# Optimization experiments

Hardware: AMD Instinct MI355X
Metric: run time of the kernel (lower is better)

## Reference

```python
import jax, jax.numpy as jnp
import numpy as np

B, V, FIN, H = 200, 40, 16, 128
NSW = 12          # switch edges
NE = 40           # regular edges
M = NE + NSW      # 52 total edges
MLP_HID = 1024
OUT = M + V + NSW # 104


def _build_graph():
    rng = np.random.default_rng(0)
    pairs = set()
    while len(pairs) < M:
        i, j = map(int, rng.integers(0, V, 2))
        if i < j:
            pairs.add((i, j))
    pairs = sorted(pairs)
    reg = np.array(pairs[:NE], np.int64)   # (NE,2)
    sw = np.array(pairs[NE:], np.int64)    # (NSW,2) row-major sorted, matches torch.nonzero order
    edges = np.concatenate([reg, sw], 0)   # switch edges last, matching graph_topo layout
    A = np.zeros((V, M), np.float32)
    A[edges[:, 0], np.arange(M)] = 1.0
    A[edges[:, 1], np.arange(M)] = -1.0
    return reg, sw, A


def setup_inputs():
    key = jax.random.key(0)
    ks = jax.random.split(key, 16)
    reg, sw, A = _build_graph()
    ei = jnp.broadcast_to(jnp.asarray(reg.T)[None], (B, 2, NE))
    si = jnp.broadcast_to(jnp.asarray(sw.T)[None], (B, 2, NSW))

    def w(k, shp, fan):
        return jax.random.normal(k, shp, jnp.float32) / np.sqrt(fan)

    return {
        'x_mod': jax.random.normal(ks[0], (B, V, FIN), jnp.float32),
        'ei': ei, 'si': si, 'A_inc': jnp.asarray(A),
        'embed': w(ks[1], (2, FIN), 1.0),
        'WU0': w(ks[2], (FIN, H), FIN), 'WV0': w(ks[3], (FIN, H), FIN),
        'WA0': w(ks[4], (FIN, H), FIN), 'WB0': w(ks[5], (FIN, H), FIN),
        'WC0': w(ks[6], (FIN, H), FIN),
        'WU1': w(ks[7], (H, H), H), 'WV1': w(ks[8], (H, H), H),
        'WA1': w(ks[9], (H, H), H), 'WB1': w(ks[10], (H, H), H),
        'WC1': w(ks[11], (H, H), H),
        'W1': w(ks[12], ((NSW + V) * H, MLP_HID), (NSW + V) * H),
        'b1': jnp.zeros((MLP_HID,), jnp.float32),
        'W2': w(ks[13], (MLP_HID, OUT), MLP_HID),
        'b2': jnp.zeros((OUT,), jnp.float32),
    }


def _layer(x, s, adj, smask, WU, WV, WA, WB, WC, residual):
    Ux = x @ WU
    Vx = x @ WV
    # gate features over dense VxV switch grid: e_ij = A s_ij + B x_i + C x_j
    e = jnp.einsum('bijf,fh->bijh', s, WA) + (x @ WB)[:, :, None, :] + (x @ WC)[:, None, :, :]
    gates = jax.nn.sigmoid(e) * smask[..., None]
    msg_edges = jnp.einsum('bij,bjh->bih', adj, Vx)   # regular-edge aggregation
    msg_sw = jnp.einsum('bijh,bjh->bih', gates, Vx)   # gated switch aggregation
    xh = jax.nn.relu(Ux + msg_edges + msg_sw)
    sh = jax.nn.relu(e)
    if residual:
        xh = x + xh
        sh = s + sh
    return xh, sh


def reference(x_mod, ei, si, A_inc, embed, WU0, WV0, WA0, WB0, WC0,
              WU1, WV1, WA1, WB1, WC1, W1, b1, W2, b2):
    i_sw, j_sw = si[0, 0], si[0, 1]   # switch indices (shared across batch)
    i_e, j_e = ei[0, 0], ei[0, 1]
    S = jnp.zeros((V, V), bool).at[i_sw, j_sw].set(True)   # upper-tri switch mask
    smask = jnp.broadcast_to(S, (B, V, V)).astype(x_mod.dtype)
    s0 = embed[S.astype(jnp.int32)]                        # (V,V,FIN) edge embedding
    s = jnp.broadcast_to(s0[None], (B, V, V, FIN))
    adj1 = jnp.zeros((V, V), x_mod.dtype).at[i_e, j_e].set(1.0)
    adj = jnp.broadcast_to((adj1 + adj1.T)[None], (B, V, V))
    x, s = _layer(x_mod, s, adj, smask, WU0, WV0, WA0, WB0, WC0, residual=False)
    x, s = _layer(x, s, adj, smask, WU1, WV1, WA1, WB1, WC1, residual=True)
    switches = s[:, i_sw, j_sw, :]                         # (B,NSW,H) irregular gather (torch.nonzero path)
    mlp_in = jnp.concatenate([switches.reshape(B, -1), x.reshape(B, -1)], axis=1)
    out = jax.nn.relu(mlp_in @ W1 + b1) @ W2 + b2          # (B,OUT)
    p_switch = jax.nn.sigmoid(out[:, -NSW:])
    graph_topo = jnp.ones((B, M), out.dtype).at[:, M - NSW:].set(p_switch)
    v = out[:, M:M + V].at[:, 0].set(1.0)
    p_fc = graph_topo * out[:, :M]
    q_fc = graph_topo * (v @ A_inc)                        # per-edge voltage difference flow
    pg = x_mod[:, :, 0] + jnp.einsum('vm,bm->bv', A_inc, p_fc)  # power balance completion
    qg = x_mod[:, :, 1] + jnp.einsum('vm,bm->bv', A_inc, q_fc)
    z = jnp.concatenate([p_fc, v, graph_topo], axis=1)     # (B, 2M+V)
    zc = jnp.concatenate([q_fc, pg, qg], axis=1)           # (B, M+2V)
    return z, zc
```

## Files before the change

### kernel.cpp

```cpp
#include <hip/hip_runtime.h>
#include <math.h>

#define B       200
#define V       40
#define FIN     16
#define H       128
#define NSW     12
#define NE      40
#define M       52
#define MLP_HID 1024
#define OUTD    104
#define MLP_IN  6656
#define ZDIM    144
#define ZCDIM   132
#define NCH     13
#define X1LD    136
#define MAXD    16

typedef __attribute__((ext_vector_type(8))) short bf16x8;
typedef __attribute__((ext_vector_type(4))) float f32x4;

__device__ __forceinline__ float sigmoidf(float x) {
    return 1.0f / (1.0f + expf(-x));
}
__device__ __forceinline__ unsigned short f2b(float x) {
    unsigned int u = __float_as_uint(x);
    u += 0x7fffu + ((u >> 16) & 1u);
    return (unsigned short)(u >> 16);
}
__device__ __forceinline__ float b2f(unsigned short s) {
    return __uint_as_float(((unsigned int)s) << 16);
}

__global__ __launch_bounds__(256) void k_prep(
        const float* __restrict__ WU0, const float* __restrict__ WV0,
        const float* __restrict__ WB0, const float* __restrict__ WC0,
        const float* __restrict__ WU1, const float* __restrict__ WV1,
        const float* __restrict__ WB1, const float* __restrict__ WC1,
        const float* __restrict__ WA1, const float* __restrict__ W2,
        unsigned short* __restrict__ W0t, unsigned short* __restrict__ Wt640,
        unsigned short* __restrict__ W2t) {
    int bx = blockIdx.x, tid = threadIdx.x;
    if (bx < 64) {
        int o0 = bx * 2048 + tid * 8;
#pragma unroll
        for (int i = 0; i < 8; ++i) {
            int o = o0 + i; int col = o >> 10, k = o & 1023;
            W2t[o] = (col < OUTD) ? f2b(W2[(size_t)k * OUTD + col]) : (unsigned short)0;
        }
    } else if (bx < 104) {
        int o0 = (bx - 64) * 2048 + tid * 8;
#pragma unroll
        for (int i = 0; i < 8; ++i) {
            int o = o0 + i; int col = o >> 7, f = o & 127;
            int m = col >> 7, hh = col & 127;
            const float* Ws = (m == 0) ? WU1 : (m == 1) ? WV1 : (m == 2) ? WB1
                            : (m == 3) ? WC1 : WA1;
            Wt640[o] = f2b(Ws[f * H + hh]);
        }
    } else {
        int o0 = (bx - 104) * 2048 + tid * 8;
#pragma unroll
        for (int i = 0; i < 8; ++i) {
            int o = o0 + i; int col = o >> 5, k = o & 31;
            int m = col >> 7, hh = col & 127;
            const float* Ws = (m == 0) ? WU0 : (m == 1) ? WV0 : (m == 2) ? WB0 : WC0;
            W0t[o] = (k < FIN) ? f2b(Ws[k * H + hh]) : (unsigned short)0;
        }
    }
}

__global__ __launch_bounds__(512) void k_gnn(const float* __restrict__ x,
        const int* __restrict__ ei, const int* __restrict__ si,
        const float* __restrict__ embed, const float* __restrict__ WA0,
        const unsigned short* __restrict__ W0t,
        const unsigned short* __restrict__ Wt640,
        unsigned short* __restrict__ Abf) {
    int b = blockIdx.x, tid = threadIdx.x;
    __shared__ unsigned short xb[48 * 40];
    __shared__ unsigned short uvbc[V * 512];
    __shared__ unsigned short x1l[64 * X1LD];
    __shared__ float gL[NSW * H];
    __shared__ float sA1l[NSW * H];
    __shared__ int   nbr[V][MAXD];
    __shared__ int   deg[V];

    int h = tid & 127, sub = tid >> 7;
    int lane = tid & 63, wv = tid >> 6;
    int lr = lane & 15, lk = lane >> 4;
    int n0w = wv * 64;

    for (int o = tid; o < 48 * 32; o += 512) {
        int r = o >> 5, k = o & 31;
        float v = (r < V && k < FIN) ? x[(size_t)b * V * FIN + r * FIN + k] : 0.f;
        xb[r * 40 + k] = f2b(v);
    }
    if (tid < V) deg[tid] = 0;
    for (int o = tid; o < 12 * 128; o += 512) {
        int rr = o >> 7;
        int row = (rr < 8) ? 40 + rr : 60 + (rr - 8);
        x1l[row * X1LD + (o & 127)] = 0;
    }
    __syncthreads();

    if (tid < NE) {
        int i = ei[tid], j = ei[NE + tid];
        int p = atomicAdd(&deg[i], 1); if (p < MAXD) nbr[i][p] = j;
        int q = atomicAdd(&deg[j], 1); if (q < MAXD) nbr[j][q] = i;
    } else if (tid < NE + NSW) {
        int k = tid - NE;
        int i = si[k], j = si[NSW + k];
        int p = atomicAdd(&deg[i], 1); if (p < MAXD) nbr[i][p] = j | ((k + 1) << 8);
    }
    {
        f32x4 acc[3][4];
#pragma unroll
        for (int rf = 0; rf < 3; ++rf)
#pragma unroll
            for (int cf = 0; cf < 4; ++cf) acc[rf][cf] = (f32x4){0.f, 0.f, 0.f, 0.f};
        int kseg = lk * 8;
        bf16x8 a0 = *(const bf16x8*)&xb[lr * 40 + kseg];
        bf16x8 a1 = *(const bf16x8*)&xb[(16 + lr) * 40 + kseg];
        bf16x8 a2 = *(const bf16x8*)&xb[(32 + lr) * 40 + kseg];
#pragma unroll
        for (int cf = 0; cf < 4; ++cf) {
            bf16x8 bf = *(const bf16x8*)&W0t[(n0w + cf * 16 + lr) * 32 + kseg];
            acc[0][cf] = __builtin_amdgcn_mfma_f32_16x16x32_bf16(a0, bf, acc[0][cf], 0, 0, 0);
            acc[1][cf] = __builtin_amdgcn_mfma_f32_16x16x32_bf16(a1, bf, acc[1][cf], 0, 0, 0);
            acc[2][cf] = __builtin_amdgcn_mfma_f32_16x16x32_bf16(a2, bf, acc[2][cf], 0, 0, 0);
        }
#pragma unroll
        for (int rf = 0; rf < 3; ++rf)
#pragma unroll
            for (int cf = 0; cf < 4; ++cf)
#pragma unroll
                for (int r = 0; r < 4; ++r) {
                    int row = rf * 16 + lk * 4 + r;
                    if (row < V) uvbc[row * 512 + n0w + cf * 16 + lr] = f2b(acc[rf][cf][r]);
                }
    }
    __syncthreads();

    {
        float sA0 = 0.f;
#pragma unroll
        for (int f = 0; f < FIN; ++f) sA0 += embed[FIN + f] * WA0[f * H + h];
        for (int k = sub; k < NSW; k += 4) {
            int i = si[k], j = si[NSW + k];
            float e0 = sA0 + b2f(uvbc[i * 512 + 256 + h]) + b2f(uvbc[j * 512 + 384 + h]);
            gL[k * H + h] = sigmoidf(e0);
            x1l[(48 + k) * X1LD + h] = f2b(fmaxf(e0, 0.f));
        }
    }
    __syncthreads();

    for (int i = sub * 10; i < sub * 10 + 10; ++i) {
        float acc = b2f(uvbc[i * 512 + h]);
        int d = deg[i]; if (d > MAXD) d = MAXD;
        for (int p = 0; p < d; ++p) {
            int ent = nbr[i][p];
            float vv = b2f(uvbc[(ent & 255) * 512 + 128 + h]);
            int g = ent >> 8;
            if (g) vv *= gL[(g - 1) * H + h];
            acc += vv;
        }
        x1l[i * X1LD + h] = f2b(fmaxf(acc, 0.f));
    }
    __syncthreads();

    {
        f32x4 acc[3][4], accs = (f32x4){0.f, 0.f, 0.f, 0.f};
#pragma unroll
        for (int rf = 0; rf < 3; ++rf)
#pragma unroll
            for (int cf = 0; cf < 4; ++cf) acc[rf][cf] = (f32x4){0.f, 0.f, 0.f, 0.f};
#pragma unroll
        for (int kk = 0; kk < 4; ++kk) {
            int kseg = kk * 32 + lk * 8;
            bf16x8 a0 = *(const bf16x8*)&x1l[lr * X1LD + kseg];
            bf16x8 a1 = *(const bf16x8*)&x1l[(16 + lr) * X1LD + kseg];
            bf16x8 a2 = *(const bf16x8*)&x1l[(32 + lr) * X1LD + kseg];
            bf16x8 as = *(const bf16x8*)&x1l[(48 + lr) * X1LD + kseg];
#pragma unroll
            for (int cf = 0; cf < 4; ++cf) {
                bf16x8 bf = *(const bf16x8*)&Wt640[(size_t)(n0w + cf * 16 + lr) * H + kseg];
                acc[0][cf] = __builtin_amdgcn_mfma_f32_16x16x32_bf16(a0, bf, acc[0][cf], 0, 0, 0);
                acc[1][cf] = __builtin_amdgcn_mfma_f32_16x16x32_bf16(a1, bf, acc[1][cf], 0, 0, 0);
                acc[2][cf] = __builtin_amdgcn_mfma_f32_16x16x32_bf16(a2, bf, acc[2][cf], 0, 0, 0);
            }
            bf16x8 bs = *(const bf16x8*)&Wt640[(size_t)(512 + wv * 16 + lr) * H + kseg];
            accs = __builtin_amdgcn_mfma_f32_16x16x32_bf16(as, bs, accs, 0, 0, 0);
        }
#pragma unroll
        for (int rf = 0; rf < 3; ++rf)
#pragma unroll
            for (int cf = 0; cf < 4; ++cf)
#pragma unroll
                for (int r = 0; r < 4; ++r) {
                    int row = rf * 16 + lk * 4 + r;
                    if (row < V) uvbc[row * 512 + n0w + cf * 16 + lr] = f2b(acc[rf][cf][r]);
                }
#pragma unroll
        for (int r = 0; r < 4; ++r) {
            int sr = lk * 4 + r;
            if (sr < NSW) sA1l[sr * H + wv * 16 + lr] = accs[r];
        }
    }
    __syncthreads();

    for (int k = sub; k < NSW; k += 4) {
        int i = si[k], j = si[NSW + k];
        float e1 = sA1l[k * H + h] + b2f(uvbc[i * 512 + 256 + h]) + b2f(uvbc[j * 512 + 384 + h]);
        gL[k * H + h] = sigmoidf(e1);
        float s1 = b2f(x1l[(48 + k) * X1LD + h]);
        Abf[(size_t)b * MLP_IN + k * H + h] = f2b(s1 + fmaxf(e1, 0.f));
    }
    __syncthreads();

    for (int i = sub * 10; i < sub * 10 + 10; ++i) {
        float acc = b2f(uvbc[i * 512 + h]);
        int d = deg[i]; if (d > MAXD) d = MAXD;
        for (int p = 0; p < d; ++p) {
            int ent = nbr[i][p];
            float vv = b2f(uvbc[(ent & 255) * 512 + 128 + h]);
            int g = ent >> 8;
            if (g) vv *= gL[(g - 1) * H + h];
            acc += vv;
        }
        float x2 = b2f(x1l[i * X1LD + h]) + fmaxf(acc, 0.f);
        Abf[(size_t)b * MLP_IN + NSW * H + i * H + h] = f2b(x2);
    }
}

__global__ __launch_bounds__(256) void k_mlp(const unsigned short* __restrict__ A,
        const float* __restrict__ W1, float* __restrict__ partial) {
    const int NK = 16;
    int tid = threadIdx.x;
    int lane = tid & 63, wvv = tid >> 6;
    int wr = (wvv >> 1) * 32, wc = (wvv & 1) * 32;
    int n0 = blockIdx.x * 64, m0 = blockIdx.y * 64;
    int kbase = blockIdx.z * NK * 32;

    __shared__ __align__(16) unsigned short a_lds[64 * 40];
    __shared__ __align__(16) unsigned short b_lds[64 * 40];

    f32x4 acc00 = {0,0,0,0}, acc01 = {0,0,0,0}, acc10 = {0,0,0,0}, acc11 = {0,0,0,0};

    int srow = tid >> 2, sseg = tid & 3;
    const int4* gA = (const int4*)(A + (size_t)(m0 + srow) * MLP_IN + kbase + sseg * 8);
    int lwsA = srow * 40 + sseg * 8;

    int bcol = tid & 63, bkg = tid >> 6;
    const float* gW = W1 + (size_t)(kbase + bkg * 8) * MLP_HID + n0 + bcol;
    int lwsB = bcol * 40 + bkg * 8;

    int a_off = (wr + (lane & 15)) * 40 + (lane >> 4) * 8;
    int b_off = (wc + (lane & 15)) * 40 + (lane >> 4) * 8;

    int4 ra = gA[0];
    float rfv[8];
#pragma unroll
    for (int i = 0; i < 8; ++i) rfv[i] = gW[(size_t)i * MLP_HID];

    for (int kk = 0; kk < NK; ++kk) {
        *(int4*)&a_lds[lwsA] = ra;
        union { unsigned short us[8]; int4 v; } pk;
#pragma unroll
        for (int i = 0; i < 8; ++i) pk.us[i] = f2b(rfv[i]);
        *(int4*)&b_lds[lwsB] = pk.v;
        __syncthreads();
        if (kk + 1 < NK) {
            ra = gA[(kk + 1) * 4];
            const float* g2 = gW + (size_t)(kk + 1) * 32 * MLP_HID;
#pragma unroll
            for (int i = 0; i < 8; ++i) rfv[i] = g2[(size_t)i * MLP_HID];
        }
        bf16x8 a0 = *(const bf16x8*)&a_lds[a_off];
        bf16x8 a1 = *(const bf16x8*)&a_lds[a_off + 16 * 40];
        bf16x8 b0 = *(const bf16x8*)&b_lds[b_off];
        bf16x8 b1 = *(const bf16x8*)&b_lds[b_off + 16 * 40];
        acc00 = __builtin_amdgcn_mfma_f32_16x16x32_bf16(a0, b0, acc00, 0, 0, 0);
        acc01 = __builtin_amdgcn_mfma_f32_16x16x32_bf16(a0, b1, acc01, 0, 0, 0);
        acc10 = __builtin_amdgcn_mfma_f32_16x16x32_bf16(a1, b0, acc10, 0, 0, 0);
        acc11 = __builtin_amdgcn_mfma_f32_16x16x32_bf16(a1, b1, acc11, 0, 0, 0);
        __syncthreads();
    }

    int crow = (lane >> 4) * 4, ccol = lane & 15;
    int row0 = m0 + wr + crow, row1 = row0 + 16;
    int col0 = n0 + wc + ccol, col1 = col0 + 16;
    float* dst = partial + (size_t)blockIdx.z * 256 * MLP_HID;
#pragma unroll
    for (int r = 0; r < 4; ++r) {
        dst[(size_t)(row0 + r) * MLP_HID + col0] = acc00[r];
        dst[(size_t)(row0 + r) * MLP_HID + col1] = acc01[r];
        dst[(size_t)(row1 + r) * MLP_HID + col0] = acc10[r];
        dst[(size_t)(row1 + r) * MLP_HID + col1] = acc11[r];
    }
}

template<int MODE>
__global__ __launch_bounds__(256) void k_gemm(const unsigned short* __restrict__ A,
        const unsigned short* __restrict__ Bt, void* __restrict__ Cout,
        int K, int nk, int ldc) {
    int tid = threadIdx.x;
    int lane = tid & 63, wv = tid >> 6;
    int wr = (wv >> 1) * 32, wc = (wv & 1) * 32;
    int n0 = blockIdx.x * 64, m0 = blockIdx.y * 64;
    size_t kbase = (size_t)blockIdx.z * nk * 32;

    __shared__ __align__(16) unsigned short a_lds[64 * 40];
    __shared__ __align__(16) unsigned short b_lds[64 * 40];

    f32x4 acc00 = {0,0,0,0}, acc01 = {0,0,0,0}, acc10 = {0,0,0,0}, acc11 = {0,0,0,0};

    int srow = tid >> 2, sseg = tid & 3;
    const int4* gA = (const int4*)(A + (size_t)(m0 + srow) * K + kbase + sseg * 8);
    const int4* gB = (const int4*)(Bt + (size_t)(n0 + srow) * K + kbase + sseg * 8);
    int lws = srow * 40 + sseg * 8;

    int a_off = (wr + (lane & 15)) * 40 + (lane >> 4) * 8;
    int b_off = (wc + (lane & 15)) * 40 + (lane >> 4) * 8;

    int4 ra = gA[0], rb = gB[0];
    for (int kk = 0; kk < nk; ++kk) {
        *(int4*)&a_lds[lws] = ra;
        *(int4*)&b_lds[lws] = rb;
        __syncthreads();
        if (kk + 1 < nk) { ra = gA[(kk + 1) * 4]; rb = gB[(kk + 1) * 4]; }
        bf16x8 a0 = *(const bf16x8*)&a_lds[a_off];
        bf16x8 a1 = *(const bf16x8*)&a_lds[a_off + 16 * 40];
        bf16x8 b0 = *(const bf16x8*)&b_lds[b_off];
        bf16x8 b1 = *(const bf16x8*)&b_lds[b_off + 16 * 40];
        acc00 = __builtin_amdgcn_mfma_f32_16x16x32_bf16(a0, b0, acc00, 0, 0, 0);
        acc01 = __builtin_amdgcn_mfma_f32_16x16x32_bf16(a0, b1, acc01, 0, 0, 0);
        acc10 = __builtin_amdgcn_mfma_f32_16x16x32_bf16(a1, b0, acc10, 0, 0, 0);
        acc11 = __builtin_amdgcn_mfma_f32_16x16x32_bf16(a1, b1, acc11, 0, 0, 0);
        __syncthreads();
    }

    int crow = (lane >> 4) * 4, ccol = lane & 15;
    int row0 = m0 + wr + crow, row1 = row0 + 16;
    int col0 = n0 + wc + ccol, col1 = col0 + 16;
    float* dst = (float*)Cout + (size_t)blockIdx.z * (gridDim.y * 64) * ldc;
#pragma unroll
    for (int r = 0; r < 4; ++r) {
        dst[(size_t)(row0 + r) * ldc + col0] = acc00[r];
        dst[(size_t)(row0 + r) * ldc + col1] = acc01[r];
        dst[(size_t)(row1 + r) * ldc + col0] = acc10[r];
        dst[(size_t)(row1 + r) * ldc + col1] = acc11[r];
    }
}

__global__ void k_mred(const float* __restrict__ partial, const float* __restrict__ b1,
                       unsigned short* __restrict__ hiddenb) {
    int i = blockIdx.x * 256 + threadIdx.x;
    float s = b1[i & (MLP_HID - 1)];
#pragma unroll
    for (int z = 0; z < NCH; ++z) s += partial[(size_t)z * 256 * MLP_HID + i];
    hiddenb[i] = f2b(fmaxf(s, 0.f));
}

__global__ __launch_bounds__(128) void k_fin(const float* __restrict__ partial2,
        const float* __restrict__ b2, const float* __restrict__ A,
        const float* __restrict__ x_mod, float* __restrict__ outp) {
    int b = blockIdx.x;
    int tid = threadIdx.x;
    __shared__ float o[OUTD];
    __shared__ float gt[M], vv[V], pfc[M], qfc[M];

    if (tid < OUTD) {
        float s = b2[tid];
#pragma unroll
        for (int z = 0; z < 4; ++z) s += partial2[(size_t)z * 256 * 128 + b * 128 + tid];
        o[tid] = s;
    }
    __syncthreads();

    if (tid < M) {
        float g = (tid < M - NSW) ? 1.0f : sigmoidf(o[M + V + (tid - (M - NSW))]);
        gt[tid] = g;
        pfc[tid] = g * o[tid];
    }
    if (tid < V) vv[tid] = (tid == 0) ? 1.0f : o[M + tid];
    __syncthreads();

    if (tid < M) {
        float acc = 0.f;
        for (int x = 0; x < V; ++x) acc += vv[x] * A[x * M + tid];
        qfc[tid] = gt[tid] * acc;
    }
    __syncthreads();

    float* zb = outp + (size_t)b * ZDIM;
    if (tid < M) zb[tid] = pfc[tid];
    if (tid < V) zb[M + tid] = vv[tid];
    if (tid < M) zb[M + V + tid] = gt[tid];

    float* zcb = outp + (size_t)B * ZDIM + (size_t)b * ZCDIM;
    if (tid < M) zcb[tid] = qfc[tid];
    if (tid < V) {
        float accp = 0.f, accq = 0.f;
        for (int m = 0; m < M; ++m) {
            float a = A[tid * M + m];
            accp += a * pfc[m];
            accq += a * qfc[m];
        }
        zcb[M + tid]     = x_mod[(size_t)(b * V + tid) * FIN + 0] + accp;
        zcb[M + V + tid] = x_mod[(size_t)(b * V + tid) * FIN + 1] + accq;
    }
}

extern "C" void kernel_launch(void* const* d_in, const int* in_sizes, int n_in,
                              void* d_out, int out_size, void* d_ws, size_t ws_size,
                              hipStream_t stream) {
    const float* x_mod = (const float*)d_in[0];
    const int*   ei    = (const int*)d_in[1];
    const int*   si    = (const int*)d_in[2];
    const float* A     = (const float*)d_in[3];
    const float* embed = (const float*)d_in[4];
    const float* WU0   = (const float*)d_in[5];
    const float* WV0   = (const float*)d_in[6];
    const float* WA0   = (const float*)d_in[7];
    const float* WB0   = (const float*)d_in[8];
    const float* WC0   = (const float*)d_in[9];
    const float* WU1   = (const float*)d_in[10];
    const float* WV1   = (const float*)d_in[11];
    const float* WA1   = (const float*)d_in[12];
    const float* WB1   = (const float*)d_in[13];
    const float* WC1   = (const float*)d_in[14];
    const float* W1    = (const float*)d_in[15];
    const float* b1    = (const float*)d_in[16];
    const float* W2    = (const float*)d_in[17];
    const float* b2    = (const float*)d_in[18];
    float* out = (float*)d_out;

    char* ws = (char*)d_ws;
    unsigned short* W0t      = (unsigned short*)(ws + 0);
    unsigned short* Wt640    = (unsigned short*)(ws + 32768);
    unsigned short* W2t      = (unsigned short*)(ws + 196608);
    unsigned short* Abf      = (unsigned short*)(ws + 458752);
    float*          partialM = (float*)(ws + 3866624);
    unsigned short* hiddenb  = (unsigned short*)(ws + 17498112);
    float*          partial2 = (float*)(ws + 18022400);

    k_prep<<<112, 256, 0, stream>>>(WU0, WV0, WB0, WC0, WU1, WV1, WB1, WC1, WA1, W2,
                                    W0t, Wt640, W2t);
    k_gnn<<<B, 512, 0, stream>>>(x_mod, ei, si, embed, WA0, W0t, Wt640, Abf);
    k_mlp<<<dim3(16, 4, NCH), 256, 0, stream>>>(Abf, W1, partialM);
    k_mred<<<256 * MLP_HID / 256, 256, 0, stream>>>(partialM, b1, hiddenb);
    k_gemm<2><<<dim3(2, 4, 4), 256, 0, stream>>>(hiddenb, W2t, partial2, MLP_HID, 8, 128);
    k_fin<<<B, 128, 0, stream>>>(partial2, b2, A, x_mod, out);
}
```

Before: 56.48 us.

## Fuse split-K reduction, second MLP GEMM and finalize into one kernel

Replaces the three tail kernels (partial-sum reduction with bias+ReLU, the MFMA GEMM for W2, and the finalize step) with a single per-batch kernel. Each block reduces its row of hidden partials into LDS as bf16, then computes the 104 outputs with a scalar dot product over W2t split across two threads per column, then runs the existing finalize logic. This removes two kernel launches and the global round-trips for the hidden and partial2 buffers. In exchange the W2 GEMM moves from MFMA to scalar FMA, and every block rereads the whole W2t matrix.

```diff
diff --git a/kernel.cpp b/kernel.cpp
--- a/kernel.cpp
+++ b/kernel.cpp
@@ -299,82 +299,43 @@
     }
 }
 
-template<int MODE>
-__global__ __launch_bounds__(256) void k_gemm(const unsigned short* __restrict__ A,
-        const unsigned short* __restrict__ Bt, void* __restrict__ Cout,
-        int K, int nk, int ldc) {
-    int tid = threadIdx.x;
-    int lane = tid & 63, wv = tid >> 6;
-    int wr = (wv >> 1) * 32, wc = (wv & 1) * 32;
-    int n0 = blockIdx.x * 64, m0 = blockIdx.y * 64;
-    size_t kbase = (size_t)blockIdx.z * nk * 32;
-
-    __shared__ __align__(16) unsigned short a_lds[64 * 40];
-    __shared__ __align__(16) unsigned short b_lds[64 * 40];
-
-    f32x4 acc00 = {0,0,0,0}, acc01 = {0,0,0,0}, acc10 = {0,0,0,0}, acc11 = {0,0,0,0};
-
-    int srow = tid >> 2, sseg = tid & 3;
-    const int4* gA = (const int4*)(A + (size_t)(m0 + srow) * K + kbase + sseg * 8);
-    const int4* gB = (const int4*)(Bt + (size_t)(n0 + srow) * K + kbase + sseg * 8);
-    int lws = srow * 40 + sseg * 8;
-
-    int a_off = (wr + (lane & 15)) * 40 + (lane >> 4) * 8;
-    int b_off = (wc + (lane & 15)) * 40 + (lane >> 4) * 8;
-
-    int4 ra = gA[0], rb = gB[0];
-    for (int kk = 0; kk < nk; ++kk) {
-        *(int4*)&a_lds[lws] = ra;
-        *(int4*)&b_lds[lws] = rb;
-        __syncthreads();
-        if (kk + 1 < nk) { ra = gA[(kk + 1) * 4]; rb = gB[(kk + 1) * 4]; }
-        bf16x8 a0 = *(const bf16x8*)&a_lds[a_off];
-        bf16x8 a1 = *(const bf16x8*)&a_lds[a_off + 16 * 40];
-        bf16x8 b0 = *(const bf16x8*)&b_lds[b_off];
-        bf16x8 b1 = *(const bf16x8*)&b_lds[b_off + 16 * 40];
-        acc00 = __builtin_amdgcn_mfma_f32_16x16x32_bf16(a0, b0, acc00, 0, 0, 0);
-        acc01 = __builtin_amdgcn_mfma_f32_16x16x32_bf16(a0, b1, acc01, 0, 0, 0);
-        acc10 = __builtin_amdgcn_mfma_f32_16x16x32_bf16(a1, b0, acc10, 0, 0, 0);
-        acc11 = __builtin_amdgcn_mfma_f32_16x16x32_bf16(a1, b1, acc11, 0, 0, 0);
-        __syncthreads();
-    }
-
-    int crow = (lane >> 4) * 4, ccol = lane & 15;
-    int row0 = m0 + wr + crow, row1 = row0 + 16;
-    int col0 = n0 + wc + ccol, col1 = col0 + 16;
-    float* dst = (float*)Cout + (size_t)blockIdx.z * (gridDim.y * 64) * ldc;
-#pragma unroll
-    for (int r = 0; r < 4; ++r) {
-        dst[(size_t)(row0 + r) * ldc + col0] = acc00[r];
-        dst[(size_t)(row0 + r) * ldc + col1] = acc01[r];
-        dst[(size_t)(row1 + r) * ldc + col0] = acc10[r];
-        dst[(size_t)(row1 + r) * ldc + col1] = acc11[r];
-    }
-}
-
-__global__ void k_mred(const float* __restrict__ partial, const float* __restrict__ b1,
-                       unsigned short* __restrict__ hiddenb) {
-    int i = blockIdx.x * 256 + threadIdx.x;
-    float s = b1[i & (MLP_HID - 1)];
-#pragma unroll
-    for (int z = 0; z < NCH; ++z) s += partial[(size_t)z * 256 * MLP_HID + i];
-    hiddenb[i] = f2b(fmaxf(s, 0.f));
-}
-
-__global__ __launch_bounds__(128) void k_fin(const float* __restrict__ partial2,
-        const float* __restrict__ b2, const float* __restrict__ A,
+__global__ __launch_bounds__(256) void k_fin2(const float* __restrict__ partialM,
+        const float* __restrict__ b1, const unsigned short* __restrict__ W2t,
+        const float* __restrict__ b2, const float* __restrict__ Ainc,
         const float* __restrict__ x_mod, float* __restrict__ outp) {
     int b = blockIdx.x;
     int tid = threadIdx.x;
+    __shared__ __align__(16) unsigned short hid[MLP_HID];
+    __shared__ float oacc[OUTD][2];
     __shared__ float o[OUTD];
     __shared__ float gt[M], vv[V], pfc[M], qfc[M];
 
-    if (tid < OUTD) {
-        float s = b2[tid];
-#pragma unroll
-        for (int z = 0; z < 4; ++z) s += partial2[(size_t)z * 256 * 128 + b * 128 + tid];
-        o[tid] = s;
-    }
+    for (int c = tid; c < MLP_HID; c += 256) {
+        float s = b1[c];
+        const float* p = partialM + (size_t)b * MLP_HID + c;
+#pragma unroll
+        for (int z = 0; z < NCH; ++z) s += p[(size_t)z * 256 * MLP_HID];
+        hid[c] = f2b(fmaxf(s, 0.f));
+    }
+    __syncthreads();
+
+    if (tid < 2 * OUTD) {
+        int col = tid >> 1, half = tid & 1;
+        const unsigned short* wrow = W2t + (size_t)col * MLP_HID + half * 512;
+        const unsigned short* hrow = hid + half * 512;
+        float acc = 0.f;
+#pragma unroll 4
+        for (int k8 = 0; k8 < 64; ++k8) {
+            bf16x8 hv = *(const bf16x8*)&hrow[k8 * 8];
+            bf16x8 wv = *(const bf16x8*)&wrow[k8 * 8];
+#pragma unroll
+            for (int i = 0; i < 8; ++i)
+                acc += b2f((unsigned short)hv[i]) * b2f((unsigned short)wv[i]);
+        }
+        oacc[col][half] = acc;
+    }
+    __syncthreads();
+    if (tid < OUTD) o[tid] = b2[tid] + oacc[tid][0] + oacc[tid][1];
     __syncthreads();
 
     if (tid < M) {
@@ -387,7 +348,7 @@
 
     if (tid < M) {
         float acc = 0.f;
-        for (int x = 0; x < V; ++x) acc += vv[x] * A[x * M + tid];
+        for (int xx = 0; xx < V; ++xx) acc += vv[xx] * Ainc[xx * M + tid];
         qfc[tid] = gt[tid] * acc;
     }
     __syncthreads();
@@ -401,10 +362,10 @@
     if (tid < M) zcb[tid] = qfc[tid];
     if (tid < V) {
         float accp = 0.f, accq = 0.f;
-        for (int m = 0; m < M; ++m) {
-            float a = A[tid * M + m];
-            accp += a * pfc[m];
-            accq += a * qfc[m];
+        for (int mm = 0; mm < M; ++mm) {
+            float a = Ainc[tid * M + mm];
+            accp += a * pfc[mm];
+            accq += a * qfc[mm];
         }
         zcb[M + tid]     = x_mod[(size_t)(b * V + tid) * FIN + 0] + accp;
         zcb[M + V + tid] = x_mod[(size_t)(b * V + tid) * FIN + 1] + accq;
@@ -417,7 +378,7 @@
     const float* x_mod = (const float*)d_in[0];
     const int*   ei    = (const int*)d_in[1];
     const int*   si    = (const int*)d_in[2];
-    const float* A     = (const float*)d_in[3];
+    const float* Ainc  = (const float*)d_in[3];
     const float* embed = (const float*)d_in[4];
     const float* WU0   = (const float*)d_in[5];
     const float* WV0   = (const float*)d_in[6];
@@ -441,14 +402,10 @@
     unsigned short* W2t      = (unsigned short*)(ws + 196608);
     unsigned short* Abf      = (unsigned short*)(ws + 458752);
     float*          partialM = (float*)(ws + 3866624);
-    unsigned short* hiddenb  = (unsigned short*)(ws + 17498112);
-    float*          partial2 = (float*)(ws + 18022400);
 
     k_prep<<<112, 256, 0, stream>>>(WU0, WV0, WB0, WC0, WU1, WV1, WB1, WC1, WA1, W2,
                                     W0t, Wt640, W2t);
     k_gnn<<<B, 512, 0, stream>>>(x_mod, ei, si, embed, WA0, W0t, Wt640, Abf);
     k_mlp<<<dim3(16, 4, NCH), 256, 0, stream>>>(Abf, W1, partialM);
-    k_mred<<<256 * MLP_HID / 256, 256, 0, stream>>>(partialM, b1, hiddenb);
-    k_gemm<2><<<dim3(2, 4, 4), 256, 0, stream>>>(hiddenb, W2t, partial2, MLP_HID, 8, 128);
-    k_fin<<<B, 128, 0, stream>>>(partial2, b2, A, x_mod, out);
-}
+    k_fin2<<<B, 256, 0, stream>>>(partialM, b1, W2t, b2, Ainc, x_mod, out);
+}
```

Measured after the change: 58.10 us. 1.03x slower.
